# Optimization experiments

Measured on AMD Instinct MI355X. Metric: run time of the kernel, lower is better.

## Reference

```python
import jax, jax.numpy as jnp
import numpy as np

NI = 2048           # per-node feature dim
H = 2 * NI          # flattened per-sample GRU state (2 nodes)
BS = 4096
NO = 1
NUM_ROUNDS = 2


def setup_inputs() -> dict:
    key = jax.random.key(0)
    ks = jax.random.split(key, 8)
    s_ih = 1.0 / np.sqrt(H)
    features = jax.random.normal(ks[0], (BS, 2, NI), dtype=jnp.float32)
    # torch.nn.GRUCell(H, H): weight_ih [3H, H], weight_hh [3H, H], biases [3H]
    W_ih = jax.random.uniform(ks[1], (3 * H, H), minval=-s_ih, maxval=s_ih, dtype=jnp.float32)
    b_ih = jax.random.uniform(ks[2], (3 * H,), minval=-s_ih, maxval=s_ih, dtype=jnp.float32)
    W_hh = jax.random.uniform(ks[3], (3 * H, H), minval=-s_ih, maxval=s_ih, dtype=jnp.float32)
    b_hh = jax.random.uniform(ks[4], (3 * H,), minval=-s_ih, maxval=s_ih, dtype=jnp.float32)
    # fc = nn.Linear(2*ni, no)
    fc_w = jax.random.uniform(ks[5], (NO, H), minval=-s_ih, maxval=s_ih, dtype=jnp.float32)
    fc_b = jax.random.uniform(ks[6], (NO,), minval=-s_ih, maxval=s_ih, dtype=jnp.float32)
    return {"features": features, "W_ih": W_ih, "b_ih": b_ih,
            "W_hh": W_hh, "b_hh": b_hh, "fc_w": fc_w, "fc_b": fc_b}


def _gru_cell(x, h, W_ih, b_ih, W_hh, b_hh):
    # torch GRUCell semantics
    gi = x @ W_ih.T + b_ih              # [bs, 3H]
    gh = h @ W_hh.T + b_hh              # [bs, 3H]
    i_r, i_z, i_n = jnp.split(gi, 3, axis=-1)
    h_r, h_z, h_n = jnp.split(gh, 3, axis=-1)
    r = jax.nn.sigmoid(i_r + h_r)
    z = jax.nn.sigmoid(i_z + h_z)
    n = jnp.tanh(i_n + r * h_n)
    return (1.0 - z) * n + z * h


def reference(features, W_ih, b_ih, W_hh, b_hh, fc_w, fc_b):
    bs = features.shape[0]
    ni = features.shape[2]
    h = features.reshape(bs, -1)        # [bs, 2*ni] = node0 || node1
    for _ in range(NUM_ROUNDS):
        # fully-connected 2-node graph, sum-aggregate of neighbor messages:
        # node0 receives h1, node1 receives h0 -> x is the half-swap of h
        x = jnp.concatenate([h[:, ni:], h[:, :ni]], axis=-1)
        h = _gru_cell(x, h, W_ih, b_ih, W_hh, b_hh)
    return h @ fc_w.T + fc_b            # [bs, no]
```

## Files before the change

kernel.cpp:

```cpp
#include <hip/hip_runtime.h>


typedef __bf16 bf16x8 __attribute__((ext_vector_type(8)));
typedef float  f32x4  __attribute__((ext_vector_type(4)));
typedef unsigned short u16x4 __attribute__((ext_vector_type(4)));

#define HH    4096
#define NI_D  2048
#define N3H   12288
#define N6H   24576
#define BSZ   4096
#define BM    256
#define BN    256
#define BK    64
#define MT    (BSZ / BM)
#define NT    (N6H / BN)
#define GRID_GEMM (MT * NT)
#define NKT   (HH / BK)

#define NB_W  98304
#define NB_C  16384

__device__ __forceinline__ unsigned short f2bf(float f) {
  unsigned u = __float_as_uint(f);
  u += 0x7FFFu + ((u >> 16) & 1u);
  return (unsigned short)(u >> 16);
}
__device__ __forceinline__ float bf2f(unsigned short s) {
  return __uint_as_float(((unsigned)s) << 16);
}

__device__ __forceinline__ void gload16(const void* g, void* l) {
  void* gv = (void*)g;
  __builtin_amdgcn_global_load_lds(
      (__attribute__((address_space(1))) unsigned int*)gv,
      (__attribute__((address_space(3))) unsigned int*)l,
      16, 0, 0);
}

__global__ void __launch_bounds__(256)
prep(const float* __restrict__ Wih, const float* __restrict__ Whh,
     const float* __restrict__ feat,
     unsigned short* __restrict__ Wc, unsigned short* __restrict__ hb)
{
  int bid = blockIdx.x;
  if (bid < NB_W) {
    int idx = (bid * 256 + threadIdx.x) << 2;
    int j = idx >> 12;
    int k = idx & 4095;
    const float* src;
    if (j < N3H) src = Wih + (size_t)j * HH + ((k + NI_D) & (HH - 1));
    else         src = Whh + (size_t)(j - N3H) * HH + k;
    f32x4 v = *(const f32x4*)src;
    u16x4 o = { f2bf(v[0]), f2bf(v[1]), f2bf(v[2]), f2bf(v[3]) };
    *(u16x4*)(Wc + idx) = o;
  } else {
    int i = ((bid - NB_W) * 256 + threadIdx.x) << 2;
    f32x4 v = *(const f32x4*)(feat + i);
    u16x4 o = { f2bf(v[0]), f2bf(v[1]), f2bf(v[2]), f2bf(v[3]) };
    *(u16x4*)(hb + i) = o;
  }
}

__device__ __forceinline__ void stageA(const char* a_base, char* lds, int ldst,
                                       int d, int kt, int g) {
  int kc = (kt < NKT) ? kt : 0;
  gload16(a_base + (size_t)kc * 128 + (size_t)g * 524288,
          lds + d * 32768 + g * 8192 + ldst);
}
__device__ __forceinline__ void stageB(const char* b_base, char* lds, int ldst,
                                       int d, int kt, int g) {
  int kc = (kt < NKT) ? kt : 0;
  gload16(b_base + (size_t)kc * 128 + (size_t)g * 524288,
          lds + 65536 + d * 32768 + g * 8192 + ldst);
}

template <int MB, int NB>
__device__ __forceinline__ void mfmaQ(f32x4 (&acc)[8][4],
                                      const bf16x8 (&af)[4][2],
                                      const bf16x8 (&bf)[2][2]) {
  __builtin_amdgcn_s_setprio(1);
#pragma unroll
  for (int ks = 0; ks < 2; ++ks)
#pragma unroll
    for (int mf = 0; mf < 4; ++mf)
#pragma unroll
      for (int nf = 0; nf < 2; ++nf)
        acc[MB + mf][NB + nf] = __builtin_amdgcn_mfma_f32_16x16x32_bf16(
            af[mf][ks], bf[nf][ks], acc[MB + mf][NB + nf], 0, 0, 0);
  __builtin_amdgcn_s_setprio(0);
}

#define BAR   __builtin_amdgcn_s_barrier()
#define LGKM0 do { asm volatile("s_waitcnt lgkmcnt(0)" ::: "memory");          \
                   __builtin_amdgcn_sched_barrier(0); } while (0)

template <int D>
__device__ __forceinline__ void kblock(char* lds, const char* a_base,
                                       const char* b_base, int ldst,
                                       int aro, int bro, int offk0, int offk1,
                                       int t1, int t2, f32x4 (&acc)[8][4]) {
  const char* LA = lds + D * 32768 + aro;
  const char* LB = lds + 65536 + D * 32768 + bro;
  bf16x8 a47[4][2], a03[4][2], b01[2][2], b23[2][2];

#pragma unroll
  for (int mf = 0; mf < 4; ++mf) {
    a47[mf][0] = *(const bf16x8*)(LA + (4 + mf) * 2048 + offk0);
    a47[mf][1] = *(const bf16x8*)(LA + (4 + mf) * 2048 + offk1);
  }
#pragma unroll
  for (int nf = 0; nf < 2; ++nf) {
    b01[nf][0] = *(const bf16x8*)(LB + nf * 2048 + offk0);
    b01[nf][1] = *(const bf16x8*)(LB + nf * 2048 + offk1);
  }
  stageA(a_base, lds, ldst, D ^ 1, t1, 0);
  stageA(a_base, lds, ldst, D ^ 1, t1, 2);
  asm volatile("s_waitcnt lgkmcnt(8)" ::: "memory");
  BAR; LGKM0;
  mfmaQ<4, 0>(acc, a47, b01);
  BAR;

#pragma unroll
  for (int nf = 0; nf < 2; ++nf) {
    b23[nf][0] = *(const bf16x8*)(LB + (2 + nf) * 2048 + offk0);
    b23[nf][1] = *(const bf16x8*)(LB + (2 + nf) * 2048 + offk1);
  }
  stageA(a_base, lds, ldst, D, t2, 1);
  stageA(a_base, lds, ldst, D, t2, 3);
  BAR; LGKM0;
  mfmaQ<4, 2>(acc, a47, b23);
  BAR;

#pragma unroll
  for (int mf = 0; mf < 4; ++mf) {
    a03[mf][0] = *(const bf16x8*)(LA + mf * 2048 + offk0);
    a03[mf][1] = *(const bf16x8*)(LA + mf * 2048 + offk1);
  }
  stageB(b_base, lds, ldst, D, t2, 0);
  stageB(b_base, lds, ldst, D, t2, 1);
  BAR; LGKM0;
  mfmaQ<0, 0>(acc, a03, b01);
  BAR;

  stageB(b_base, lds, ldst, D, t2, 2);
  stageB(b_base, lds, ldst, D, t2, 3);
  BAR;
  mfmaQ<0, 2>(acc, a03, b23);
  asm volatile("s_waitcnt vmcnt(6)" ::: "memory");
  BAR;
}

__global__ void __launch_bounds__(512, 2)
gemm_bt(const unsigned short* __restrict__ A,
        const unsigned short* __restrict__ B,
        unsigned short* __restrict__ C)
{
  __shared__ alignas(16) char lds[131072];

  int bid = blockIdx.x;
  int wg  = (bid & 7) * (GRID_GEMM / 8) + (bid >> 3);
  int nt  = wg / MT;
  int mt  = wg % MT;
  int m0  = mt * BM;
  int n0  = nt * BN;

  int t  = threadIdx.x;
  int wv = t >> 6;
  int l  = t & 63;
  int wm = wv >> 2;
  int wn = wv & 3;

  int rloc   = wv * 8 + (l >> 3);
  int sg_col = ((l & 7) ^ (l >> 3)) << 4;
  const char* a_base = (const char*)A + (size_t)(m0 + rloc) * 8192 + sg_col;
  const char* b_base = (const char*)B + (size_t)(n0 + rloc) * 8192 + sg_col;
  int ldst = wv * 1024;

  int offk0 = ((l >> 4) << 4) ^ ((l & 7) << 4);
  int offk1 = offk0 ^ 64;
  int aro = (wm * 128 + (l & 15)) * 128;
  int bro = (wn * 64  + (l & 15)) * 128;

  f32x4 acc[8][4] = {};

#pragma unroll
  for (int g = 0; g < 4; ++g) stageA(a_base, lds, ldst, 0, 0, g);
#pragma unroll
  for (int g = 0; g < 4; ++g) stageB(b_base, lds, ldst, 0, 0, g);
  stageA(a_base, lds, ldst, 1, 1, 1);
  stageA(a_base, lds, ldst, 1, 1, 3);
#pragma unroll
  for (int g = 0; g < 4; ++g) stageB(b_base, lds, ldst, 1, 1, g);
  asm volatile("s_waitcnt vmcnt(6)" ::: "memory");
  BAR;

#pragma unroll 1
  for (int tt = 0; tt < NKT; tt += 2) {
    kblock<0>(lds, a_base, b_base, ldst, aro, bro, offk0, offk1,
              tt + 1, tt + 2, acc);
    kblock<1>(lds, a_base, b_base, ldst, aro, bro, offk0, offk1,
              tt + 2, tt + 3, acc);
  }
  asm volatile("s_waitcnt vmcnt(0)" ::: "memory");

  int crow = m0 + wm * 128 + ((l >> 4) << 2);
  int ccol = n0 + wn * 64 + (l & 15);
#pragma unroll
  for (int mf = 0; mf < 8; ++mf)
#pragma unroll
    for (int nf = 0; nf < 4; ++nf)
#pragma unroll
      for (int i = 0; i < 4; ++i)
        C[(size_t)(crow + mf * 16 + i) * N6H + (ccol + nf * 16)] =
            f2bf(acc[mf][nf][i]);
}

__global__ void __launch_bounds__(256)
gru1(const unsigned short* __restrict__ C, const float* __restrict__ h_old,
     const float* __restrict__ b_ih, const float* __restrict__ b_hh,
     unsigned short* __restrict__ h_bf)
{
  int idx = blockIdx.x * 256 + threadIdx.x;
  int b = idx >> 10;
  int j = (idx & 1023) << 2;
  const unsigned short* Cr = C + (size_t)b * N6H;
  u16x4 gir = *(const u16x4*)(Cr + j);
  u16x4 giz = *(const u16x4*)(Cr + HH + j);
  u16x4 gin = *(const u16x4*)(Cr + 2 * HH + j);
  u16x4 ghr = *(const u16x4*)(Cr + 3 * HH + j);
  u16x4 ghz = *(const u16x4*)(Cr + 4 * HH + j);
  u16x4 ghn = *(const u16x4*)(Cr + 5 * HH + j);
  f32x4 bir = *(const f32x4*)(b_ih + j);
  f32x4 biz = *(const f32x4*)(b_ih + HH + j);
  f32x4 bin = *(const f32x4*)(b_ih + 2 * HH + j);
  f32x4 bhr = *(const f32x4*)(b_hh + j);
  f32x4 bhz = *(const f32x4*)(b_hh + HH + j);
  f32x4 bhn = *(const f32x4*)(b_hh + 2 * HH + j);
  f32x4 ho  = *(const f32x4*)(h_old + (size_t)b * HH + j);
  u16x4 hb;
#pragma unroll
  for (int e = 0; e < 4; ++e) {
    float r = 1.f / (1.f + expf(-(bf2f(gir[e]) + bir[e] + bf2f(ghr[e]) + bhr[e])));
    float z = 1.f / (1.f + expf(-(bf2f(giz[e]) + biz[e] + bf2f(ghz[e]) + bhz[e])));
    float n = tanhf(bf2f(gin[e]) + bin[e] + r * (bf2f(ghn[e]) + bhn[e]));
    hb[e] = f2bf((1.f - z) * n + z * ho[e]);
  }
  *(u16x4*)(h_bf + (size_t)b * HH + j) = hb;
}

__global__ void __launch_bounds__(256)
gru2_fc(const unsigned short* __restrict__ C,
        const unsigned short* __restrict__ h_old_bf,
        const float* __restrict__ b_ih, const float* __restrict__ b_hh,
        const float* __restrict__ fcw, const float* __restrict__ fcb,
        float* __restrict__ out)
{
  int idx = blockIdx.x * 256 + threadIdx.x;
  int b = idx >> 10;
  int j = (idx & 1023) << 2;
  const unsigned short* Cr = C + (size_t)b * N6H;
  u16x4 gir = *(const u16x4*)(Cr + j);
  u16x4 giz = *(const u16x4*)(Cr + HH + j);
  u16x4 gin = *(const u16x4*)(Cr + 2 * HH + j);
  u16x4 ghr = *(const u16x4*)(Cr + 3 * HH + j);
  u16x4 ghz = *(const u16x4*)(Cr + 4 * HH + j);
  u16x4 ghn = *(const u16x4*)(Cr + 5 * HH + j);
  f32x4 bir = *(const f32x4*)(b_ih + j);
  f32x4 biz = *(const f32x4*)(b_ih + HH + j);
  f32x4 bin = *(const f32x4*)(b_ih + 2 * HH + j);
  f32x4 bhr = *(const f32x4*)(b_hh + j);
  f32x4 bhz = *(const f32x4*)(b_hh + HH + j);
  f32x4 bhn = *(const f32x4*)(b_hh + 2 * HH + j);
  u16x4 hob = *(const u16x4*)(h_old_bf + (size_t)b * HH + j);
  f32x4 fw  = *(const f32x4*)(fcw + j);
  float s = 0.f;
#pragma unroll
  for (int e = 0; e < 4; ++e) {
    float r = 1.f / (1.f + expf(-(bf2f(gir[e]) + bir[e] + bf2f(ghr[e]) + bhr[e])));
    float z = 1.f / (1.f + expf(-(bf2f(giz[e]) + biz[e] + bf2f(ghz[e]) + bhz[e])));
    float n = tanhf(bf2f(gin[e]) + bin[e] + r * (bf2f(ghn[e]) + bhn[e]));
    float h = (1.f - z) * n + z * bf2f(hob[e]);
    s += h * fw[e];
  }
#pragma unroll
  for (int off = 32; off > 0; off >>= 1) s += __shfl_down(s, off);
  __shared__ float red[4];
  if ((threadIdx.x & 63) == 0) red[threadIdx.x >> 6] = s;
  __syncthreads();
  if (threadIdx.x == 0) {
    float v = red[0] + red[1] + red[2] + red[3];
    if ((blockIdx.x & 3) == 0) v += fcb[0];
    atomicAdd(&out[b], v);
  }
}

extern "C" void kernel_launch(void* const* d_in, const int* in_sizes, int n_in,
                              void* d_out, int out_size, void* d_ws, size_t ws_size,
                              hipStream_t stream)
{
  const float* feat = (const float*)d_in[0];
  const float* Wih  = (const float*)d_in[1];
  const float* bih  = (const float*)d_in[2];
  const float* Whh  = (const float*)d_in[3];
  const float* bhh  = (const float*)d_in[4];
  const float* fcw  = (const float*)d_in[5];
  const float* fcb  = (const float*)d_in[6];
  float* out = (float*)d_out;

  char* ws = (char*)d_ws;
  unsigned short* Wc   = (unsigned short*)ws;
  unsigned short* Cbuf = (unsigned short*)(ws + 201326592);
  unsigned short* hb   = (unsigned short*)(ws + 402653184);

  hipMemsetAsync(out, 0, (size_t)out_size * sizeof(float), stream);
  prep<<<NB_W + NB_C, 256, 0, stream>>>(Wih, Whh, feat, Wc, hb);

  gemm_bt<<<GRID_GEMM, 512, 0, stream>>>(hb, Wc, Cbuf);
  gru1<<<16384, 256, 0, stream>>>(Cbuf, feat, bih, bhh, hb);

  gemm_bt<<<GRID_GEMM, 512, 0, stream>>>(hb, Wc, Cbuf);
  gru2_fc<<<16384, 256, 0, stream>>>(Cbuf, hb, bih, bhh, fcw, fcb, out);
}
```

Before: 1.546 ms.

## Software-pipeline LDS fragment loads across k-blocks with ping-pong register buffers

Restructures the GEMM inner k-block so the LDS reads for the next block's first quadrant (a47/b01) are issued during the last MFMA quadrant of the current block. Each quadrant's fragment loads are overlapped with the previous quadrant's MFMAs, and the barrier/waitcnt placement is reshuffled so the vmcnt waits sit after the MFMAs. The goal is to hide LDS read latency behind matrix-core work. In exchange it adds two sets of double-buffered fragment registers, raising VGPR pressure under the 2-wave-per-SIMD launch bound and risking spills or lower occupancy.

```diff
diff --git a/kernel.cpp b/kernel.cpp
--- a/kernel.cpp
+++ b/kernel.cpp
@@ -92,62 +92,70 @@
 }
 
 #define BAR   __builtin_amdgcn_s_barrier()
-#define LGKM0 do { asm volatile("s_waitcnt lgkmcnt(0)" ::: "memory");          \
-                   __builtin_amdgcn_sched_barrier(0); } while (0)
+#define SB    __builtin_amdgcn_sched_barrier(0)
+#define LGKM0 do { asm volatile("s_waitcnt lgkmcnt(0)" ::: "memory"); SB; } while (0)
+#define VM6   asm volatile("s_waitcnt vmcnt(6)" ::: "memory")
 
 template <int D>
 __device__ __forceinline__ void kblock(char* lds, const char* a_base,
                                        const char* b_base, int ldst,
                                        int aro, int bro, int offk0, int offk1,
-                                       int t1, int t2, f32x4 (&acc)[8][4]) {
-  const char* LA = lds + D * 32768 + aro;
-  const char* LB = lds + 65536 + D * 32768 + bro;
-  bf16x8 a47[4][2], a03[4][2], b01[2][2], b23[2][2];
-
-#pragma unroll
-  for (int mf = 0; mf < 4; ++mf) {
-    a47[mf][0] = *(const bf16x8*)(LA + (4 + mf) * 2048 + offk0);
-    a47[mf][1] = *(const bf16x8*)(LA + (4 + mf) * 2048 + offk1);
-  }
-#pragma unroll
-  for (int nf = 0; nf < 2; ++nf) {
-    b01[nf][0] = *(const bf16x8*)(LB + nf * 2048 + offk0);
-    b01[nf][1] = *(const bf16x8*)(LB + nf * 2048 + offk1);
-  }
-  stageA(a_base, lds, ldst, D ^ 1, t1, 0);
-  stageA(a_base, lds, ldst, D ^ 1, t1, 2);
-  asm volatile("s_waitcnt lgkmcnt(8)" ::: "memory");
-  BAR; LGKM0;
-  mfmaQ<4, 0>(acc, a47, b01);
-  BAR;
-
+                                       int t1, int t2, f32x4 (&acc)[8][4],
+                                       bf16x8 (&a47c)[4][2], bf16x8 (&b01c)[2][2],
+                                       bf16x8 (&a47n)[4][2], bf16x8 (&b01n)[2][2]) {
+  const char* LA  = lds + D * 32768 + aro;
+  const char* LB  = lds + 65536 + D * 32768 + bro;
+  const char* LAn = lds + (D ^ 1) * 32768 + aro;
+  const char* LBn = lds + 65536 + (D ^ 1) * 32768 + bro;
+  bf16x8 a03[4][2], b23[2][2];
+
+  LGKM0;
 #pragma unroll
   for (int nf = 0; nf < 2; ++nf) {
     b23[nf][0] = *(const bf16x8*)(LB + (2 + nf) * 2048 + offk0);
     b23[nf][1] = *(const bf16x8*)(LB + (2 + nf) * 2048 + offk1);
   }
-  stageA(a_base, lds, ldst, D, t2, 1);
-  stageA(a_base, lds, ldst, D, t2, 3);
-  BAR; LGKM0;
-  mfmaQ<4, 2>(acc, a47, b23);
-  BAR;
-
+  stageA(a_base, lds, ldst, D ^ 1, t1, 0);
+  stageA(a_base, lds, ldst, D ^ 1, t1, 2);
+  SB;
+  mfmaQ<4, 0>(acc, a47c, b01c);
+  VM6;
+  BAR;
+
+  LGKM0;
 #pragma unroll
   for (int mf = 0; mf < 4; ++mf) {
     a03[mf][0] = *(const bf16x8*)(LA + mf * 2048 + offk0);
     a03[mf][1] = *(const bf16x8*)(LA + mf * 2048 + offk1);
   }
+  stageA(a_base, lds, ldst, D, t2, 1);
+  stageA(a_base, lds, ldst, D, t2, 3);
+  SB;
+  mfmaQ<4, 2>(acc, a47c, b23);
+  BAR;
+
+  LGKM0;
   stageB(b_base, lds, ldst, D, t2, 0);
   stageB(b_base, lds, ldst, D, t2, 1);
-  BAR; LGKM0;
-  mfmaQ<0, 0>(acc, a03, b01);
-  BAR;
-
+  SB;
+  mfmaQ<0, 0>(acc, a03, b01c);
+  VM6;
+  BAR;
+
+#pragma unroll
+  for (int mf = 0; mf < 4; ++mf) {
+    a47n[mf][0] = *(const bf16x8*)(LAn + (4 + mf) * 2048 + offk0);
+    a47n[mf][1] = *(const bf16x8*)(LAn + (4 + mf) * 2048 + offk1);
+  }
+#pragma unroll
+  for (int nf = 0; nf < 2; ++nf) {
+    b01n[nf][0] = *(const bf16x8*)(LBn + nf * 2048 + offk0);
+    b01n[nf][1] = *(const bf16x8*)(LBn + nf * 2048 + offk1);
+  }
   stageB(b_base, lds, ldst, D, t2, 2);
   stageB(b_base, lds, ldst, D, t2, 3);
-  BAR;
+  SB;
   mfmaQ<0, 2>(acc, a03, b23);
-  asm volatile("s_waitcnt vmcnt(6)" ::: "memory");
   BAR;
 }
 
@@ -183,6 +191,7 @@
   int bro = (wn * 64  + (l & 15)) * 128;
 
   f32x4 acc[8][4] = {};
+  bf16x8 a47A[4][2], b01A[2][2], a47B[4][2], b01B[2][2];
 
 #pragma unroll
   for (int g = 0; g < 4; ++g) stageA(a_base, lds, ldst, 0, 0, g);
@@ -194,15 +203,29 @@
   for (int g = 0; g < 4; ++g) stageB(b_base, lds, ldst, 1, 1, g);
   asm volatile("s_waitcnt vmcnt(6)" ::: "memory");
   BAR;
+  {
+    const char* LA0 = lds + aro;
+    const char* LB0 = lds + 65536 + bro;
+#pragma unroll
+    for (int mf = 0; mf < 4; ++mf) {
+      a47A[mf][0] = *(const bf16x8*)(LA0 + (4 + mf) * 2048 + offk0);
+      a47A[mf][1] = *(const bf16x8*)(LA0 + (4 + mf) * 2048 + offk1);
+    }
+#pragma unroll
+    for (int nf = 0; nf < 2; ++nf) {
+      b01A[nf][0] = *(const bf16x8*)(LB0 + nf * 2048 + offk0);
+      b01A[nf][1] = *(const bf16x8*)(LB0 + nf * 2048 + offk1);
+    }
+  }
 
 #pragma unroll 1
   for (int tt = 0; tt < NKT; tt += 2) {
     kblock<0>(lds, a_base, b_base, ldst, aro, bro, offk0, offk1,
-              tt + 1, tt + 2, acc);
+              tt + 1, tt + 2, acc, a47A, b01A, a47B, b01B);
     kblock<1>(lds, a_base, b_base, ldst, aro, bro, offk0, offk1,
-              tt + 2, tt + 3, acc);
-  }
-  asm volatile("s_waitcnt vmcnt(0)" ::: "memory");
+              tt + 2, tt + 3, acc, a47B, b01B, a47A, b01A);
+  }
+  asm volatile("s_waitcnt vmcnt(0) lgkmcnt(0)" ::: "memory");
 
   int crow = m0 + wm * 128 + ((l >> 4) << 2);
   int ccol = n0 + wn * 64 + (l & 15);
```

After: 1.503 ms. -2.8%, faster.

## Pre-swizzle weights into MFMA fragment layout and load B directly to registers

Applied to the files above, without the earlier changes.

The prep kernel now writes the bf16 weight matrix in a fragment-ordered layout, so each wave can read its B operands for the MFMA straight from global memory into registers. This drops B staging through LDS, halves the LDS footprint and removes some barriers. The k-loop is restructured to prefetch A and B fragments across phases with vmcnt-based waits. The risk is that B global-load latency is now exposed in the MFMA pipeline, and the B tile is fetched separately by each of the two wm waves instead of being shared through LDS.

```diff
diff --git a/kernel.cpp b/kernel.cpp
--- a/kernel.cpp
+++ b/kernel.cpp
@@ -4,6 +4,7 @@
 typedef __bf16 bf16x8 __attribute__((ext_vector_type(8)));
 typedef float  f32x4  __attribute__((ext_vector_type(4)));
 typedef unsigned short u16x4 __attribute__((ext_vector_type(4)));
+typedef unsigned short u16x8 __attribute__((ext_vector_type(8)));
 
 #define HH    4096
 #define NI_D  2048
@@ -18,7 +19,7 @@
 #define GRID_GEMM (MT * NT)
 #define NKT   (HH / BK)
 
-#define NB_W  98304
+#define NB_W  49152
 #define NB_C  16384
 
 __device__ __forceinline__ unsigned short f2bf(float f) {
@@ -41,21 +42,26 @@
 __global__ void __launch_bounds__(256)
 prep(const float* __restrict__ Wih, const float* __restrict__ Whh,
      const float* __restrict__ feat,
-     unsigned short* __restrict__ Wc, unsigned short* __restrict__ hb)
+     unsigned short* __restrict__ Wf, unsigned short* __restrict__ hb)
 {
   int bid = blockIdx.x;
+  int t = threadIdx.x;
   if (bid < NB_W) {
-    int idx = (bid * 256 + threadIdx.x) << 2;
-    int j = idx >> 12;
-    int k = idx & 4095;
+    int jg  = bid >> 5;
+    int kcg = bid & 31;
+    int j   = jg * 16 + (t & 15);
+    int kc  = kcg * 16 + (t >> 4);
+    int k   = kc * 8;
     const float* src;
     if (j < N3H) src = Wih + (size_t)j * HH + ((k + NI_D) & (HH - 1));
     else         src = Whh + (size_t)(j - N3H) * HH + k;
-    f32x4 v = *(const f32x4*)src;
-    u16x4 o = { f2bf(v[0]), f2bf(v[1]), f2bf(v[2]), f2bf(v[3]) };
-    *(u16x4*)(Wc + idx) = o;
+    f32x4 v0 = *(const f32x4*)src;
+    f32x4 v1 = *(const f32x4*)(src + 4);
+    u16x8 o = { f2bf(v0[0]), f2bf(v0[1]), f2bf(v0[2]), f2bf(v0[3]),
+                f2bf(v1[0]), f2bf(v1[1]), f2bf(v1[2]), f2bf(v1[3]) };
+    *(u16x8*)(Wf + (size_t)jg * 65536 + kc * 128 + (t & 15) * 8) = o;
   } else {
-    int i = ((bid - NB_W) * 256 + threadIdx.x) << 2;
+    int i = ((bid - NB_W) * 256 + t) << 2;
     f32x4 v = *(const f32x4*)(feat + i);
     u16x4 o = { f2bf(v[0]), f2bf(v[1]), f2bf(v[2]), f2bf(v[3]) };
     *(u16x4*)(hb + i) = o;
@@ -68,12 +74,6 @@
   gload16(a_base + (size_t)kc * 128 + (size_t)g * 524288,
           lds + d * 32768 + g * 8192 + ldst);
 }
-__device__ __forceinline__ void stageB(const char* b_base, char* lds, int ldst,
-                                       int d, int kt, int g) {
-  int kc = (kt < NKT) ? kt : 0;
-  gload16(b_base + (size_t)kc * 128 + (size_t)g * 524288,
-          lds + 65536 + d * 32768 + g * 8192 + ldst);
-}
 
 template <int MB, int NB>
 __device__ __forceinline__ void mfmaQ(f32x4 (&acc)[8][4],
@@ -92,44 +92,30 @@
 }
 
 #define BAR   __builtin_amdgcn_s_barrier()
-#define LGKM0 do { asm volatile("s_waitcnt lgkmcnt(0)" ::: "memory");          \
-                   __builtin_amdgcn_sched_barrier(0); } while (0)
+#define SB    __builtin_amdgcn_sched_barrier(0)
+#define LGKM0 do { asm volatile("s_waitcnt lgkmcnt(0)" ::: "memory"); SB; } while (0)
+#define VM12  asm volatile("s_waitcnt vmcnt(12)" ::: "memory")
 
 template <int D>
 __device__ __forceinline__ void kblock(char* lds, const char* a_base,
-                                       const char* b_base, int ldst,
-                                       int aro, int bro, int offk0, int offk1,
-                                       int t1, int t2, f32x4 (&acc)[8][4]) {
-  const char* LA = lds + D * 32768 + aro;
-  const char* LB = lds + 65536 + D * 32768 + bro;
-  bf16x8 a47[4][2], a03[4][2], b01[2][2], b23[2][2];
-
-#pragma unroll
-  for (int mf = 0; mf < 4; ++mf) {
-    a47[mf][0] = *(const bf16x8*)(LA + (4 + mf) * 2048 + offk0);
-    a47[mf][1] = *(const bf16x8*)(LA + (4 + mf) * 2048 + offk1);
-  }
-#pragma unroll
-  for (int nf = 0; nf < 2; ++nf) {
-    b01[nf][0] = *(const bf16x8*)(LB + nf * 2048 + offk0);
-    b01[nf][1] = *(const bf16x8*)(LB + nf * 2048 + offk1);
-  }
-  stageA(a_base, lds, ldst, D ^ 1, t1, 0);
-  stageA(a_base, lds, ldst, D ^ 1, t1, 2);
-  asm volatile("s_waitcnt lgkmcnt(8)" ::: "memory");
-  BAR; LGKM0;
+                                       const char* wfk, int ldst,
+                                       int aro, int offk0, int offk1,
+                                       int tcur, f32x4 (&acc)[8][4],
+                                       bf16x8 (&a47)[4][2], bf16x8 (&a03)[4][2],
+                                       bf16x8 (&b01)[2][2], bf16x8 (&b23)[2][2]) {
+  const char* LA  = lds + D * 32768 + aro;
+  const char* LAn = lds + (D ^ 1) * 32768 + aro;
+
+#pragma unroll
+  for (int nf = 0; nf < 2; ++nf)
+#pragma unroll
+    for (int kh = 0; kh < 2; ++kh)
+      b23[nf][kh] = *(const bf16x8*)(wfk + (2 + nf) * 131072 + kh * 1024);
+  stageA(a_base, lds, ldst, D ^ 1, tcur + 1, 0);
+  stageA(a_base, lds, ldst, D ^ 1, tcur + 1, 2);
+  LGKM0;
   mfmaQ<4, 0>(acc, a47, b01);
-  BAR;
-
-#pragma unroll
-  for (int nf = 0; nf < 2; ++nf) {
-    b23[nf][0] = *(const bf16x8*)(LB + (2 + nf) * 2048 + offk0);
-    b23[nf][1] = *(const bf16x8*)(LB + (2 + nf) * 2048 + offk1);
-  }
-  stageA(a_base, lds, ldst, D, t2, 1);
-  stageA(a_base, lds, ldst, D, t2, 3);
-  BAR; LGKM0;
-  mfmaQ<4, 2>(acc, a47, b23);
+  VM12;
   BAR;
 
 #pragma unroll
@@ -137,26 +123,38 @@
     a03[mf][0] = *(const bf16x8*)(LA + mf * 2048 + offk0);
     a03[mf][1] = *(const bf16x8*)(LA + mf * 2048 + offk1);
   }
-  stageB(b_base, lds, ldst, D, t2, 0);
-  stageB(b_base, lds, ldst, D, t2, 1);
-  BAR; LGKM0;
+  stageA(a_base, lds, ldst, D, tcur + 2, 1);
+  stageA(a_base, lds, ldst, D, tcur + 2, 3);
+  SB;
+  mfmaQ<4, 2>(acc, a47, b23);
+  BAR;
+
+  LGKM0;
   mfmaQ<0, 0>(acc, a03, b01);
-  BAR;
-
-  stageB(b_base, lds, ldst, D, t2, 2);
-  stageB(b_base, lds, ldst, D, t2, 3);
-  BAR;
+  VM12;
+  BAR;
+
+#pragma unroll
+  for (int mf = 0; mf < 4; ++mf) {
+    a47[mf][0] = *(const bf16x8*)(LAn + (4 + mf) * 2048 + offk0);
+    a47[mf][1] = *(const bf16x8*)(LAn + (4 + mf) * 2048 + offk1);
+  }
+#pragma unroll
+  for (int nf = 0; nf < 2; ++nf)
+#pragma unroll
+    for (int kh = 0; kh < 2; ++kh)
+      b01[nf][kh] = *(const bf16x8*)(wfk + 2048 + nf * 131072 + kh * 1024);
+  SB;
   mfmaQ<0, 2>(acc, a03, b23);
-  asm volatile("s_waitcnt vmcnt(6)" ::: "memory");
   BAR;
 }
 
 __global__ void __launch_bounds__(512, 2)
 gemm_bt(const unsigned short* __restrict__ A,
-        const unsigned short* __restrict__ B,
+        const unsigned short* __restrict__ Wf,
         unsigned short* __restrict__ C)
 {
-  __shared__ alignas(16) char lds[131072];
+  __shared__ alignas(16) char lds[65536];
 
   int bid = blockIdx.x;
   int wg  = (bid & 7) * (GRID_GEMM / 8) + (bid >> 3);
@@ -174,35 +172,47 @@
   int rloc   = wv * 8 + (l >> 3);
   int sg_col = ((l & 7) ^ (l >> 3)) << 4;
   const char* a_base = (const char*)A + (size_t)(m0 + rloc) * 8192 + sg_col;
-  const char* b_base = (const char*)B + (size_t)(n0 + rloc) * 8192 + sg_col;
   int ldst = wv * 1024;
 
   int offk0 = ((l >> 4) << 4) ^ ((l & 7) << 4);
   int offk1 = offk0 ^ 64;
   int aro = (wm * 128 + (l & 15)) * 128;
-  int bro = (wn * 64  + (l & 15)) * 128;
+
+  const char* wfb = (const char*)Wf +
+                    ((size_t)(n0 >> 4) + wn * 4) * 131072 + (size_t)l * 16;
 
   f32x4 acc[8][4] = {};
+  bf16x8 a47[4][2], a03[4][2], b01[2][2], b23[2][2];
 
 #pragma unroll
   for (int g = 0; g < 4; ++g) stageA(a_base, lds, ldst, 0, 0, g);
-#pragma unroll
-  for (int g = 0; g < 4; ++g) stageB(b_base, lds, ldst, 0, 0, g);
   stageA(a_base, lds, ldst, 1, 1, 1);
   stageA(a_base, lds, ldst, 1, 1, 3);
 #pragma unroll
-  for (int g = 0; g < 4; ++g) stageB(b_base, lds, ldst, 1, 1, g);
+  for (int nf = 0; nf < 2; ++nf)
+#pragma unroll
+    for (int kh = 0; kh < 2; ++kh)
+      b01[nf][kh] = *(const bf16x8*)(wfb + nf * 131072 + kh * 1024);
   asm volatile("s_waitcnt vmcnt(6)" ::: "memory");
   BAR;
+  {
+    const char* LA0 = lds + aro;
+#pragma unroll
+    for (int mf = 0; mf < 4; ++mf) {
+      a47[mf][0] = *(const bf16x8*)(LA0 + (4 + mf) * 2048 + offk0);
+      a47[mf][1] = *(const bf16x8*)(LA0 + (4 + mf) * 2048 + offk1);
+    }
+  }
 
 #pragma unroll 1
   for (int tt = 0; tt < NKT; tt += 2) {
-    kblock<0>(lds, a_base, b_base, ldst, aro, bro, offk0, offk1,
-              tt + 1, tt + 2, acc);
-    kblock<1>(lds, a_base, b_base, ldst, aro, bro, offk0, offk1,
-              tt + 2, tt + 3, acc);
-  }
-  asm volatile("s_waitcnt vmcnt(0)" ::: "memory");
+    const char* wfk = wfb + (size_t)tt * 2048;
+    kblock<0>(lds, a_base, wfk, ldst, aro, offk0, offk1,
+              tt, acc, a47, a03, b01, b23);
+    kblock<1>(lds, a_base, wfk + 2048, ldst, aro, offk0, offk1,
+              tt + 1, acc, a47, a03, b01, b23);
+  }
+  asm volatile("s_waitcnt vmcnt(0) lgkmcnt(0)" ::: "memory");
 
   int crow = m0 + wm * 128 + ((l >> 4) << 2);
   int ccol = n0 + wn * 64 + (l & 15);
@@ -309,16 +319,16 @@
   float* out = (float*)d_out;
 
   char* ws = (char*)d_ws;
-  unsigned short* Wc   = (unsigned short*)ws;
+  unsigned short* Wf   = (unsigned short*)ws;
   unsigned short* Cbuf = (unsigned short*)(ws + 201326592);
   unsigned short* hb   = (unsigned short*)(ws + 402653184);
 
   hipMemsetAsync(out, 0, (size_t)out_size * sizeof(float), stream);
-  prep<<<NB_W + NB_C, 256, 0, stream>>>(Wih, Whh, feat, Wc, hb);
-
-  gemm_bt<<<GRID_GEMM, 512, 0, stream>>>(hb, Wc, Cbuf);
+  prep<<<NB_W + NB_C, 256, 0, stream>>>(Wih, Whh, feat, Wf, hb);
+
+  gemm_bt<<<GRID_GEMM, 512, 0, stream>>>(hb, Wf, Cbuf);
   gru1<<<16384, 256, 0, stream>>>(Cbuf, feat, bih, bhh, hb);
 
-  gemm_bt<<<GRID_GEMM, 512, 0, stream>>>(hb, Wc, Cbuf);
+  gemm_bt<<<GRID_GEMM, 512, 0, stream>>>(hb, Wf, Cbuf);
   gru2_fc<<<16384, 256, 0, stream>>>(Cbuf, hb, bih, bhh, fcw, fcb, out);
 }
```

Measured after the change: 1.770 ms. 14.4% more time.
